# Kernel tuning notes

Hardware: AMD Instinct MI355X
Metric: run time of the kernel (lower is better)

The kernel has to match this reference:

```python
import jax, jax.numpy as jnp
import numpy as np

RADIUS = 2  # half window; original kernel truncates the spatial Gaussian at ~2.5*sigma


def setup_inputs() -> dict:
    key = jax.random.key(0)
    input_img = jax.random.normal(key, (2, 1, 128, 128, 128), dtype=jnp.float32)
    return {
        "input_img": input_img,
        "sigma_x": jnp.float32(1.0),
        "sigma_y": jnp.float32(1.0),
        "sigma_z": jnp.float32(1.0),
        "color_sigma": jnp.float32(0.5),
    }


def reference(input_img, sigma_x, sigma_y, sigma_z, color_sigma):
    # 3D bilateral filter: out(i) = sum_k w_spatial(k) * w_range(x_i, x_k) * x_k / sum_k w
    R = RADIUS
    pad = [(0, 0), (0, 0), (R, R), (R, R), (R, R)]
    xp = jnp.pad(input_img, pad)                       # zero-padded volume
    mp = jnp.pad(jnp.ones_like(input_img), pad)        # validity mask (out-of-bounds taps excluded)

    offs = np.array([(dx, dy, dz)
                     for dx in range(-R, R + 1)
                     for dy in range(-R, R + 1)
                     for dz in range(-R, R + 1)], dtype=np.int32)  # (K,3), K=125
    d2 = jnp.asarray(offs.astype(np.float32) ** 2)     # squared offsets (K,3)
    w_sp = jnp.exp(-(d2[:, 0] / (2.0 * sigma_x ** 2)
                     + d2[:, 1] / (2.0 * sigma_y ** 2)
                     + d2[:, 2] / (2.0 * sigma_z ** 2)))  # (K,)
    starts = jnp.asarray(offs + R)                     # slice starts into the padded volume

    inv_2cs2 = 1.0 / (2.0 * color_sigma ** 2)
    shape = input_img.shape

    def body(carry, inp):
        num, den = carry
        start, ws = inp
        s = jnp.concatenate([jnp.zeros(2, jnp.int32), start])
        xk = jax.lax.dynamic_slice(xp, s, shape)       # shifted neighbor volume
        mk = jax.lax.dynamic_slice(mp, s, shape)
        w = ws * mk * jnp.exp(-(input_img - xk) ** 2 * inv_2cs2)
        return (num + w * xk, den + w), None

    zero = jnp.zeros_like(input_img)
    (num, den), _ = jax.lax.scan(body, (zero, zero), (starts, w_sp))
    return num / den
```

## Files before the change

kernel.cpp:

```cpp
#include <hip/hip_runtime.h>
#include <hip/hip_bf16.h>


#define RADIUS 2
#define N 128
#define TX 16
#define TY 8
#define TZ 8
#define PITCH (TX + 2 * RADIUS)
#define LYD (TY + 2 * RADIUS)
#define LZD (TZ + 2 * RADIUS)
#define LDS_SIZE (PITCH * LYD * LZD)

#define LOG2E 1.4426950408889634f
#define BIG 1.0e18f
#define EXP2_SCALE 8388608.0f
#define EXP2_BIAS 1065353216.0f

__global__ __launch_bounds__(256, 6) void bilateral3d_kernel(
    const float* __restrict__ in, const float* __restrict__ p_sx,
    const float* __restrict__ p_sy, const float* __restrict__ p_sz,
    const float* __restrict__ p_cs, float* __restrict__ out) {
  __shared__ float s[LDS_SIZE];

  const int tid = threadIdx.x;
  const int x0 = blockIdx.x * TX;
  const int y0 = blockIdx.y * TY;
  const int zb = blockIdx.z;
  const int z0 = (zb & 15) * TZ;
  const int b = zb >> 4;

  const float sxv = p_sx[0], syv = p_sy[0], szv = p_sz[0], csv = p_cs[0];
  const float AX2 = EXP2_SCALE * LOG2E / (2.0f * sxv * sxv);
  const float AY2 = EXP2_SCALE * LOG2E / (2.0f * syv * syv);
  const float AZ2 = EXP2_SCALE * LOG2E / (2.0f * szv * szv);
  const float AX2_4 = 4.0f * AX2;
  const float sR = __builtin_sqrtf(EXP2_SCALE * LOG2E / (2.0f * csv * csv));

  const float* vol = in + (size_t)b * (N * N * N);

  for (int i = tid; i < LDS_SIZE; i += 256) {
    int lx = i % PITCH;
    int t = i / PITCH;
    int ly = t % LYD;
    int lz = t / LYD;
    int gx = x0 + lx - RADIUS;
    int gy = y0 + ly - RADIUS;
    int gz = z0 + lz - RADIUS;
    float v = BIG;
    if ((unsigned)gx < N && (unsigned)gy < N && (unsigned)gz < N)
      v = vol[((size_t)gz * N + gy) * N + gx];
    s[i] = v * sR;
  }
  __syncthreads();

  const int ty = tid & 7;
  const int tx = (tid >> 3) & 3;
  const int tz = tid >> 5;

  const int xw = 4 * tx;

  const int cbase = ((tz + RADIUS) * LYD + (ty + RADIUS)) * PITCH + xw;
  const float4 CA = *(const float4*)&s[cbase];
  const float4 CB = *(const float4*)&s[cbase + 4];
  const float xc0 = CA.z, xc1 = CA.w, xc2 = CB.x, xc3 = CB.y;

  float n0 = 0, n1 = 0, n2 = 0, n3 = 0;
  float e0 = 0, e1 = 0, e2 = 0, e3 = 0;

#define TAP(XC, FV, CC, NN, DD)                          \
  {                                                      \
    float _t = (XC) - (FV);                              \
    float _f = fmaf(_t, -_t, (CC));                      \
    unsigned _q;                                         \
    asm("v_cvt_u32_f32 %0, %1" : "=v"(_q) : "v"(_f));    \
    float _w = __uint_as_float(_q);                      \
    DD += _w;                                            \
    NN = fmaf(_w, (FV), NN);                             \
  }

#pragma unroll 1
  for (int dz = -RADIUS; dz <= RADIUS; ++dz) {
    const float pz2 = AZ2 * (float)(dz * dz);
    const int zrow = (tz + RADIUS + dz) * LYD;
#pragma unroll
    for (int dy = -RADIUS; dy <= RADIUS; ++dy) {
      const float cc0 = EXP2_BIAS - (pz2 + AY2 * (float)(dy * dy));
      const float cm1 = cc0 - AX2;
      const float cm4 = cc0 - AX2_4;
      const int rb = (zrow + (ty + RADIUS + dy)) * PITCH + xw;
      const float4 A = *(const float4*)&s[rb];
      const float4 B = *(const float4*)&s[rb + 4];
      const float f0 = A.x, f1 = A.y, f2 = A.z, f3 = A.w;
      const float f4 = B.x, f5 = B.y, f6 = B.z, f7 = B.w;

      TAP(xc0, f0, cm4, n0, e0)
      TAP(xc1, f1, cm4, n1, e1)
      TAP(xc2, f2, cm4, n2, e2)
      TAP(xc3, f3, cm4, n3, e3)
      TAP(xc0, f1, cm1, n0, e0)
      TAP(xc1, f2, cm1, n1, e1)
      TAP(xc2, f3, cm1, n2, e2)
      TAP(xc3, f4, cm1, n3, e3)
      TAP(xc0, f2, cc0, n0, e0)
      TAP(xc1, f3, cc0, n1, e1)
      TAP(xc2, f4, cc0, n2, e2)
      TAP(xc3, f5, cc0, n3, e3)
      TAP(xc0, f3, cm1, n0, e0)
      TAP(xc1, f4, cm1, n1, e1)
      TAP(xc2, f5, cm1, n2, e2)
      TAP(xc3, f6, cm1, n3, e3)
      TAP(xc0, f4, cm4, n0, e0)
      TAP(xc1, f5, cm4, n1, e1)
      TAP(xc2, f6, cm4, n2, e2)
      TAP(xc3, f7, cm4, n3, e3)
    }
  }

  float4 r;
  r.x = n0 / (e0 * sR);
  r.y = n1 / (e1 * sR);
  r.z = n2 / (e2 * sR);
  r.w = n3 / (e3 * sR);

  const int gz = z0 + tz, gy = y0 + ty;
  *(float4*)&out[(((size_t)b * N + gz) * N + gy) * N + (x0 + xw)] = r;
}

extern "C" void kernel_launch(void* const* d_in, const int* in_sizes, int n_in,
                              void* d_out, int out_size, void* d_ws, size_t ws_size,
                              hipStream_t stream) {
  const float* in = (const float*)d_in[0];
  const float* sx = (const float*)d_in[1];
  const float* sy = (const float*)d_in[2];
  const float* sz = (const float*)d_in[3];
  const float* cs = (const float*)d_in[4];
  float* out = (float*)d_out;

  dim3 grid(N / TX, N / TY, (N / TZ) * 2);
  bilateral3d_kernel<<<grid, 256, 0, stream>>>(in, sx, sy, sz, cs, out);
}
```

Baseline: 137.3 us.

## Compute two z-outputs per thread to reuse LDS row loads

Each thread now produces two adjacent z outputs, so the z-tile doubles to 16 and the grid halves. Each loaded LDS row (float4 pair) feeds both outputs' taps across a 6-plane sweep, which cuts LDS reads per output and shrinks the halo overhead relative to the tile. The final division is replaced by a hardware reciprocal multiply. The cost is twice as many accumulator registers, fewer blocks, and slightly lower precision in the final normalization.

Result: no change. 139.6 us (+1.7%).

```diff
diff --git a/kernel.cpp b/kernel.cpp
--- a/kernel.cpp
+++ b/kernel.cpp
@@ -1,12 +1,11 @@
 #include <hip/hip_runtime.h>
-#include <hip/hip_bf16.h>
 
 
 #define RADIUS 2
 #define N 128
 #define TX 16
 #define TY 8
-#define TZ 8
+#define TZ 16
 #define PITCH (TX + 2 * RADIUS)
 #define LYD (TY + 2 * RADIUS)
 #define LZD (TZ + 2 * RADIUS)
@@ -27,8 +26,8 @@
   const int x0 = blockIdx.x * TX;
   const int y0 = blockIdx.y * TY;
   const int zb = blockIdx.z;
-  const int z0 = (zb & 15) * TZ;
-  const int b = zb >> 4;
+  const int z0 = (zb & 7) * TZ;
+  const int b = zb >> 3;
 
   const float sxv = p_sx[0], syv = p_sy[0], szv = p_sz[0], csv = p_cs[0];
   const float AX2 = EXP2_SCALE * LOG2E / (2.0f * sxv * sxv);
@@ -60,13 +59,19 @@
 
   const int xw = 4 * tx;
 
-  const int cbase = ((tz + RADIUS) * LYD + (ty + RADIUS)) * PITCH + xw;
-  const float4 CA = *(const float4*)&s[cbase];
-  const float4 CB = *(const float4*)&s[cbase + 4];
-  const float xc0 = CA.z, xc1 = CA.w, xc2 = CB.x, xc3 = CB.y;
+  const int cbaseA = ((2 * tz + RADIUS) * LYD + (ty + RADIUS)) * PITCH + xw;
+  const int cbaseB = cbaseA + LYD * PITCH;
+  const float4 CA0 = *(const float4*)&s[cbaseA];
+  const float4 CA1 = *(const float4*)&s[cbaseA + 4];
+  const float4 CB0 = *(const float4*)&s[cbaseB];
+  const float4 CB1 = *(const float4*)&s[cbaseB + 4];
+  const float a0 = CA0.z, a1 = CA0.w, a2 = CA1.x, a3 = CA1.y;
+  const float c0v = CB0.z, c1v = CB0.w, c2v = CB1.x, c3v = CB1.y;
 
-  float n0 = 0, n1 = 0, n2 = 0, n3 = 0;
-  float e0 = 0, e1 = 0, e2 = 0, e3 = 0;
+  float nA0 = 0, nA1 = 0, nA2 = 0, nA3 = 0;
+  float eA0 = 0, eA1 = 0, eA2 = 0, eA3 = 0;
+  float nB0 = 0, nB1 = 0, nB2 = 0, nB3 = 0;
+  float eB0 = 0, eB1 = 0, eB2 = 0, eB3 = 0;
 
 #define TAP(XC, FV, CC, NN, DD)                          \
   {                                                      \
@@ -79,52 +84,68 @@
     NN = fmaf(_w, (FV), NN);                             \
   }
 
+#define ROW20(C0, C1, C4, X0, X1, X2, X3, N0, N1, N2, N3, E0, E1, E2, E3) \
+  TAP(X0, f0, C4, N0, E0) TAP(X1, f1, C4, N1, E1)                          \
+  TAP(X2, f2, C4, N2, E2) TAP(X3, f3, C4, N3, E3)                          \
+  TAP(X0, f1, C1, N0, E0) TAP(X1, f2, C1, N1, E1)                          \
+  TAP(X2, f3, C1, N2, E2) TAP(X3, f4, C1, N3, E3)                          \
+  TAP(X0, f2, C0, N0, E0) TAP(X1, f3, C0, N1, E1)                          \
+  TAP(X2, f4, C0, N2, E2) TAP(X3, f5, C0, N3, E3)                          \
+  TAP(X0, f3, C1, N0, E0) TAP(X1, f4, C1, N1, E1)                          \
+  TAP(X2, f5, C1, N2, E2) TAP(X3, f6, C1, N3, E3)                          \
+  TAP(X0, f4, C4, N0, E0) TAP(X1, f5, C4, N1, E1)                          \
+  TAP(X2, f6, C4, N2, E2) TAP(X3, f7, C4, N3, E3)
+
 #pragma unroll 1
-  for (int dz = -RADIUS; dz <= RADIUS; ++dz) {
-    const float pz2 = AZ2 * (float)(dz * dz);
-    const int zrow = (tz + RADIUS + dz) * LYD;
+  for (int dzw = 0; dzw < 6; ++dzw) {
+    const float d2A = (float)((dzw - 2) * (dzw - 2));
+    const float d2B = (float)((dzw - 3) * (dzw - 3));
+    const float pz2A = AZ2 * d2A;
+    const float pz2B = AZ2 * d2B;
+    const int zrow = (2 * tz + dzw) * LYD;
+    const bool doA = (dzw <= 4);
+    const bool doB = (dzw >= 1);
 #pragma unroll
-    for (int dy = -RADIUS; dy <= RADIUS; ++dy) {
-      const float cc0 = EXP2_BIAS - (pz2 + AY2 * (float)(dy * dy));
-      const float cm1 = cc0 - AX2;
-      const float cm4 = cc0 - AX2_4;
-      const int rb = (zrow + (ty + RADIUS + dy)) * PITCH + xw;
+    for (int dy = 0; dy < 5; ++dy) {
+      const float py2 = AY2 * (float)((dy - 2) * (dy - 2));
+      const int rb = (zrow + (ty + dy)) * PITCH + xw;
       const float4 A = *(const float4*)&s[rb];
       const float4 B = *(const float4*)&s[rb + 4];
       const float f0 = A.x, f1 = A.y, f2 = A.z, f3 = A.w;
       const float f4 = B.x, f5 = B.y, f6 = B.z, f7 = B.w;
-
-      TAP(xc0, f0, cm4, n0, e0)
-      TAP(xc1, f1, cm4, n1, e1)
-      TAP(xc2, f2, cm4, n2, e2)
-      TAP(xc3, f3, cm4, n3, e3)
-      TAP(xc0, f1, cm1, n0, e0)
-      TAP(xc1, f2, cm1, n1, e1)
-      TAP(xc2, f3, cm1, n2, e2)
-      TAP(xc3, f4, cm1, n3, e3)
-      TAP(xc0, f2, cc0, n0, e0)
-      TAP(xc1, f3, cc0, n1, e1)
-      TAP(xc2, f4, cc0, n2, e2)
-      TAP(xc3, f5, cc0, n3, e3)
-      TAP(xc0, f3, cm1, n0, e0)
-      TAP(xc1, f4, cm1, n1, e1)
-      TAP(xc2, f5, cm1, n2, e2)
-      TAP(xc3, f6, cm1, n3, e3)
-      TAP(xc0, f4, cm4, n0, e0)
-      TAP(xc1, f5, cm4, n1, e1)
-      TAP(xc2, f6, cm4, n2, e2)
-      TAP(xc3, f7, cm4, n3, e3)
+      if (doA) {
+        const float cc0 = EXP2_BIAS - (pz2A + py2);
+        const float cm1 = cc0 - AX2;
+        const float cm4 = cc0 - AX2_4;
+        ROW20(cc0, cm1, cm4, a0, a1, a2, a3,
+              nA0, nA1, nA2, nA3, eA0, eA1, eA2, eA3)
+      }
+      if (doB) {
+        const float cc0 = EXP2_BIAS - (pz2B + py2);
+        const float cm1 = cc0 - AX2;
+        const float cm4 = cc0 - AX2_4;
+        ROW20(cc0, cm1, cm4, c0v, c1v, c2v, c3v,
+              nB0, nB1, nB2, nB3, eB0, eB1, eB2, eB3)
+      }
     }
   }
 
-  float4 r;
-  r.x = n0 / (e0 * sR);
-  r.y = n1 / (e1 * sR);
-  r.z = n2 / (e2 * sR);
-  r.w = n3 / (e3 * sR);
+  const float isR = 1.0f / sR;
+  float4 rA, rB;
+  rA.x = (nA0 * __builtin_amdgcn_rcpf(eA0)) * isR;
+  rA.y = (nA1 * __builtin_amdgcn_rcpf(eA1)) * isR;
+  rA.z = (nA2 * __builtin_amdgcn_rcpf(eA2)) * isR;
+  rA.w = (nA3 * __builtin_amdgcn_rcpf(eA3)) * isR;
+  rB.x = (nB0 * __builtin_amdgcn_rcpf(eB0)) * isR;
+  rB.y = (nB1 * __builtin_amdgcn_rcpf(eB1)) * isR;
+  rB.z = (nB2 * __builtin_amdgcn_rcpf(eB2)) * isR;
+  rB.w = (nB3 * __builtin_amdgcn_rcpf(eB3)) * isR;
 
-  const int gz = z0 + tz, gy = y0 + ty;
-  *(float4*)&out[(((size_t)b * N + gz) * N + gy) * N + (x0 + xw)] = r;
+  const int gy = y0 + ty;
+  const int gzA = z0 + 2 * tz;
+  const size_t obase = (((size_t)b * N + gzA) * N + gy) * N + (x0 + xw);
+  *(float4*)&out[obase] = rA;
+  *(float4*)&out[obase + (size_t)N * N] = rB;
 }
 
 extern "C" void kernel_launch(void* const* d_in, const int* in_sizes, int n_in,
```
